# Performance work log

Measured on AMD Instinct MI355X. Metric: run time of the kernel, lower is better.

The kernel has to match this reference:

```python
import jax, jax.numpy as jnp
import numpy as np

N = 100000      # num_nodes
E = 500000      # num_edges
D = 128         # memory_dim (also per-head out channels of TransformerConv)
EF = 16         # edge_feat_dim
H = 2           # heads
OUT = 64        # classifier out_channels


def setup_inputs() -> dict:
    key = jax.random.key(0)
    ks = jax.random.split(key, 24)
    g = lambda k, shape, s=0.05: (jax.random.normal(k, shape, jnp.float32) * s)
    inp = {
        "edge_index": jax.random.randint(ks[0], (2, E), 0, N, dtype=jnp.int64),
        "edge_attr": jax.random.normal(ks[1], (E, EF), jnp.float32),
        "edge_time": jax.random.uniform(ks[2], (E,), jnp.float32),
        # memory buffer (non-trainable in torch); randn so gathers are non-trivial
        "memory": g(ks[3], (N, D), 0.1),
        # MessageModule MLP: Linear(2D+EF -> D), ReLU, Linear(D -> D)
        "w1": g(ks[4], (2 * D + EF, D)), "b1": g(ks[5], (D,)),
        "w2": g(ks[6], (D, D)), "b2": g(ks[7], (D,)),
        # GRUCell(D, D): torch layout [3D, D] with gate order r,z,n
        "gru_wih": g(ks[8], (3 * D, D)), "gru_whh": g(ks[9], (3 * D, D)),
        "gru_bih": g(ks[10], (3 * D,)), "gru_bhh": g(ks[11], (3 * D,)),
        # TransformerConv(D, D, heads=H): lin_query/key/value: D -> H*D, lin_skip: D -> H*D
        "wq": g(ks[12], (D, H * D)), "bq": g(ks[13], (H * D,)),
        "wk": g(ks[14], (D, H * D)), "bk": g(ks[15], (H * D,)),
        "wv": g(ks[16], (D, H * D)), "bv": g(ks[17], (H * D,)),
        "wskip": g(ks[18], (D, H * D)), "bskip": g(ks[19], (H * D,)),
        # classifier: H*D -> OUT
        "wc": g(ks[20], (H * D, OUT)), "bc": g(ks[21], (OUT,)),
    }
    return inp


def reference(edge_index, edge_attr, edge_time, memory, w1, b1, w2, b2,
              gru_wih, gru_whh, gru_bih, gru_bhh,
              wq, bq, wk, bk, wv, bv, wskip, bskip, wc, bc):
    n_nodes = memory.shape[0]
    src, dst = edge_index[0], edge_index[1]
    # memory is a requires_grad=False parameter in torch
    mem = jax.lax.stop_gradient(memory)

    # ---- message computation (gather + MLP) ----
    src_mem = mem[src]                      # [E, D]
    dst_mem = mem[dst]                      # [E, D]
    msg_in = jnp.concatenate([src_mem, dst_mem, edge_attr], axis=-1)
    messages = jax.nn.relu(msg_in @ w1 + b1) @ w2 + b2   # [E, D]

    # ---- GRUCell memory update (torch gate order: r, z, n) ----
    gi = messages @ gru_wih.T + gru_bih     # [E, 3D]
    gh = dst_mem @ gru_whh.T + gru_bhh      # [E, 3D]
    i_r, i_z, i_n = jnp.split(gi, 3, axis=-1)
    h_r, h_z, h_n = jnp.split(gh, 3, axis=-1)
    r = jax.nn.sigmoid(i_r + h_r)
    z = jax.nn.sigmoid(i_z + h_z)
    n = jnp.tanh(i_n + r * h_n)
    new_mem = (1.0 - z) * n + z * dst_mem   # [E, D]
    # detached scatter write (memory.data[node_ids] = updated_mem.data)
    node_mem = mem.at[dst].set(jax.lax.stop_gradient(new_mem))  # [N, D]

    # ---- TransformerConv(D, D, heads=H), concat=True, root_weight=True ----
    q = (node_mem @ wq + bq).reshape(n_nodes, H, D)
    k = (node_mem @ wk + bk).reshape(n_nodes, H, D)
    v = (node_mem @ wv + bv).reshape(n_nodes, H, D)
    # per-edge attention logits, aggregated at destination node
    logits = jnp.sum(q[dst] * k[src], axis=-1) / jnp.sqrt(jnp.float32(D))  # [E, H]
    m = jax.ops.segment_max(logits, dst, num_segments=n_nodes)             # [N, H]
    ex = jnp.exp(logits - m[dst])
    s = jax.ops.segment_sum(ex, dst, num_segments=n_nodes)                 # [N, H]
    alpha = ex / (s[dst] + 1e-16)                                          # [E, H]
    agg = jax.ops.segment_sum(v[src] * alpha[..., None], dst,
                              num_segments=n_nodes)                        # [N, H, D]
    conv_out = agg.reshape(n_nodes, H * D) + node_mem @ wskip + bskip

    # ---- classifier ----
    return conv_out @ wc + bc               # [N, OUT]
```

## Files before the change

kernel.cpp:

```cpp
#include <hip/hip_runtime.h>
#include <hip/hip_bf16.h>

#define DD 128
#define EFD 16
#define HDIM 256
#define OUTD 64
#define AW 296

#define P_W1T 0
#define P_W2T 36864
#define P_WIH 53248
#define P_WHH 102400
#define P_QKV 151552
#define P_WSK 249856
#define P_WCT 282624
#define P_TOT 299008

using bf16 = __hip_bfloat16;
typedef __attribute__((ext_vector_type(8))) short fab;
typedef __attribute__((ext_vector_type(4))) float f4;

__device__ __forceinline__ float b2f(bf16 x){ return __bfloat162float(x); }
__device__ __forceinline__ bf16  f2b(float x){ return __float2bfloat16(x); }
__device__ __forceinline__ unsigned short us(bf16 x){ return *(unsigned short*)&x; }
__device__ __forceinline__ float rawbf(unsigned int u16){
  return __uint_as_float(u16 << 16);
}
__device__ __forceinline__ unsigned pk2(float a, float b){
  return (unsigned)us(f2b(a)) | ((unsigned)us(f2b(b)) << 16);
}
__device__ __forceinline__ float gw(const void* p, size_t i, int f32){
  return f32 ? ((const float*)p)[i] : b2f(((const bf16*)p)[i]);
}
__device__ __forceinline__ uint2 ld4bf(const void* base, size_t off, int f32){
  if(f32){
    float4 v = *(const float4*)((const float*)base + off);
    uint2 r;
    r.x = pk2(v.x, v.y);
    r.y = pk2(v.z, v.w);
    return r;
  }
  return *(const uint2*)((const bf16*)base + off);
}
__device__ __forceinline__ int geti(const int* ei, int is64, long long idx){
  return is64 ? ei[2*idx] : ei[(size_t)idx];
}
__device__ __forceinline__ int clampi(int x, int hi){
  return x < 0 ? 0 : (x >= hi ? hi-1 : x);
}
__device__ __forceinline__ float gru_out(float ir, float hr, float iz, float hz,
                                         float in_, float hn, float bN_i, float bN_h,
                                         float bR, float bZ, float hp, bool upd){
  if(!upd) return hp;
  float rr = 1.f/(1.f+__expf(-(ir+hr+bR)));
  float zz = 1.f/(1.f+__expf(-(iz+hz+bZ)));
  float nn = tanhf(in_+bN_i + rr*(hn+bN_h));
  return (1.f-zz)*nn + zz*hp;
}

__global__ void k_detect(const int* __restrict__ ei,
                         const unsigned short* __restrict__ mem16,
                         int* __restrict__ flags){
  __shared__ int s64, sf32;
  int t = threadIdx.x;
  if(t == 0){ s64 = 1; sf32 = 0; }
  __syncthreads();
  if(ei[2*t + 1] != 0) atomicAnd(&s64, 0);
  int cnt = 0;
  for(int i = t; i < 4096; i += 256){
    unsigned short h = mem16[2*i];
    if((h & 0x7f80u) >= 0x4000u) cnt++;
  }
  atomicAdd(&sf32, cnt);
  __syncthreads();
  if(t == 0){ flags[0] = s64; flags[1] = (sf32 > 8) ? 1 : 0; }
}

__global__ void k_init(int* winner, int* cntrp, int N){
  int i = blockIdx.x*blockDim.x + threadIdx.x;
  if(i < N) winner[i] = -1;
  if(i <= N) cntrp[i] = 0;
}

__global__ void k_winner(const int* __restrict__ ei, const int* __restrict__ flags,
                         int* winner, int* cntrp, int E, int N){
  int e = blockIdx.x*blockDim.x + threadIdx.x;
  if(e >= E) return;
  int d = clampi(geti(ei, flags[0], (long long)E + e), N);
  atomicMax(&winner[d], e);
  atomicAdd(&cntrp[d], 1);
}

__global__ void k_scanA(const int* __restrict__ cnt, int* __restrict__ bsum, int N, int P){
  __shared__ int sd[256];
  int b = blockIdx.x, t = threadIdx.x;
  int base = (b*256 + t)*P;
  int s = 0;
  for(int p=0;p<P;p++){ int i = base+p; if(i<N) s += cnt[i]; }
  sd[t] = s; __syncthreads();
  for(int off=128; off>0; off>>=1){
    if(t<off) sd[t] += sd[t+off];
    __syncthreads();
  }
  if(t==0) bsum[b] = sd[0];
}

__global__ void k_scanB(const int* __restrict__ bsum, int* __restrict__ boff,
                        int* __restrict__ rowptr, int N, int E){
  __shared__ int sd[256];
  int t = threadIdx.x;
  int v = bsum[t];
  sd[t] = v; __syncthreads();
  for(int off=1; off<256; off<<=1){
    int u = (t>=off) ? sd[t-off] : 0;
    __syncthreads();
    sd[t] += u;
    __syncthreads();
  }
  boff[t] = sd[t] - v;
  if(t==0) rowptr[N] = E;
}

__global__ void k_scanC(int* __restrict__ cntrp, const int* __restrict__ boff,
                        int* __restrict__ head, int N, int P){
  __shared__ int sd[256];
  int b = blockIdx.x, t = threadIdx.x;
  int base = (b*256 + t)*P;
  int loc[8];
  int s = 0;
  for(int p=0;p<P;p++){ int i=base+p; int cc=(i<N)?cntrp[i]:0; loc[p]=s; s+=cc; }
  sd[t]=s; __syncthreads();
  for(int off=1; off<256; off<<=1){
    int u=(t>=off)?sd[t-off]:0;
    __syncthreads(); sd[t]+=u; __syncthreads();
  }
  int start = boff[b] + sd[t] - s;
  for(int p=0;p<P;p++){
    int i=base+p;
    if(i<N){ int r = start + loc[p]; cntrp[i]=r; head[i]=r; }
  }
}

__global__ void k_scatter(const int* __restrict__ ei, const int* __restrict__ flags,
                          int* __restrict__ head, int* __restrict__ esrc, int E, int N){
  int e = blockIdx.x*256 + threadIdx.x;
  if(e >= E) return;
  int is64 = flags[0];
  int src = clampi(geti(ei, is64, e), N);
  int dst = clampi(geti(ei, is64, (long long)E + e), N);
  int slot = atomicAdd(&head[dst], 1);
  esrc[slot] = src;
}

__global__ void k_pack(const void* w1, const void* w2, const void* wih, const void* whh,
                       const void* wq, const void* wk, const void* wv,
                       const void* wsk, const void* wc,
                       const int* __restrict__ flags, bf16* __restrict__ pk){
  int i = blockIdx.x*256 + threadIdx.x;
  if(i >= P_TOT) return;
  int f = flags[1];
  float v;
  if(i < P_W2T){ int j = i/288, c = i%288; v = (c < 272) ? gw(w1,(size_t)c*DD + j, f) : 0.f; }
  else if(i < P_WIH){ int r = i - P_W2T; int j = r>>7, c = r&127; v = gw(w2,(size_t)c*DD + j, f); }
  else if(i < P_WHH){ v = gw(wih, i - P_WIH, f); }
  else if(i < P_QKV){ v = gw(whh, i - P_WHH, f); }
  else if(i < P_WSK){
    int r = i - P_QKV; int jj = r>>7, c = r&127;
    int tb = jj>>8, j = jj&255;
    const void* w = (tb==0) ? wq : ((tb==1) ? wk : wv);
    v = gw(w, (size_t)c*HDIM + j, f);
  }
  else if(i < P_WCT){ int r = i - P_WSK; int j = r>>7, c = r&127; v = gw(wsk,(size_t)c*HDIM + j, f); }
  else { int r = i - P_WCT; int o = r>>8, j = r&255; v = gw(wc,(size_t)j*OUTD + o, f); }
  pk[i] = f2b(v);
}

__global__ __launch_bounds__(512) void k_msggru_qkv(
    const int* __restrict__ ei, const void* __restrict__ eattr,
    const void* __restrict__ mem, const bf16* __restrict__ pk,
    const void* b1, const void* b2, const void* bih, const void* bhh,
    const void* bq, const void* bk, const void* bv,
    const int* __restrict__ winner, const int* __restrict__ flags,
    bf16* __restrict__ node_mem, bf16* __restrict__ qt, bf16* __restrict__ kv, int N){
  const bf16* pw1T = pk + P_W1T;
  const bf16* pw2T = pk + P_W2T;
  const bf16* pwih = pk + P_WIH;
  const bf16* pwhh = pk + P_WHH;
  __shared__ bf16 Abuf[128][AW];
  __shared__ int swin[128], ssrc[128];
  int t = threadIdx.x;
  int n0 = blockIdx.x*128;
  int f = flags[1], is64 = flags[0];
  if(t < 128){
    int n = n0 + t;
    int w = (n < N) ? winner[n] : -1;
    swin[t] = w;
    ssrc[t] = (w >= 0) ? clampi(geti(ei, is64, w), N) : 0;
  }
  __syncthreads();
  const uint2 z2 = {0u, 0u};
  for(int idx=t; idx<128*32; idx+=512){
    int i = idx>>5, c4 = (idx&31)*4;
    int w = swin[i], n = n0+i;
    uint2 sv = (w>=0) ? ld4bf(mem, (size_t)ssrc[i]*DD + c4, f) : z2;
    uint2 dv = (n<N)  ? ld4bf(mem, (size_t)n*DD + c4, f)      : z2;
    *(uint2*)&Abuf[i][c4]    = sv;
    *(uint2*)&Abuf[i][DD+c4] = dv;
  }
  for(int idx=t; idx<128*4; idx+=512){
    int i = idx>>2, c4 = (idx&3)*4;
    uint2 v = (swin[i]>=0) ? ld4bf(eattr, (size_t)swin[i]*EFD + c4, f) : z2;
    *(uint2*)&Abuf[i][256+c4] = v;
  }
  for(int idx=t; idx<128*6; idx+=512){
    int i = idx/6, c4 = 272 + (idx%6)*4;
    *(uint2*)&Abuf[i][c4] = z2;
  }
  __syncthreads();

  int lane  = t & 63;
  int wid   = t >> 6;
  int col16 = lane & 15;
  int quad  = lane >> 4;
  int q8    = quad*8;
  int ch    = wid*16 + quad*4;

  {
    uint2 hres[8];
    const bf16* wrow = pw1T + (size_t)(wid*16 + col16)*288 + q8;
    fab w[9];
    #pragma unroll
    for(int kc=0;kc<9;kc++) w[kc] = *(const fab*)(wrow + kc*32);
    float bb0 = gw(b1, ch,   f), bb1 = gw(b1, ch+1, f);
    float bb2 = gw(b1, ch+2, f), bb3 = gw(b1, ch+3, f);
    #pragma unroll
    for(int mt=0; mt<8; mt++){
      f4 acc = (f4){0.f,0.f,0.f,0.f};
      #pragma unroll
      for(int kc=0;kc<9;kc++){
        fab an = *(const fab*)&Abuf[mt*16+col16][kc*32+q8];
        acc = __builtin_amdgcn_mfma_f32_16x16x32_bf16(w[kc], an, acc, 0,0,0);
      }
      uint2 hv;
      hv.x = pk2(fmaxf(acc[0]+bb0,0.f), fmaxf(acc[1]+bb1,0.f));
      hv.y = pk2(fmaxf(acc[2]+bb2,0.f), fmaxf(acc[3]+bb3,0.f));
      hres[mt] = hv;
    }
    __syncthreads();
    #pragma unroll
    for(int mt=0; mt<8; mt++)
      *(uint2*)&Abuf[mt*16+col16][ch] = hres[mt];
    __syncthreads();
  }

  {
    uint2 mres[8];
    const bf16* wrow = pw2T + (size_t)(wid*16 + col16)*128 + q8;
    fab w[4];
    #pragma unroll
    for(int kc=0;kc<4;kc++) w[kc] = *(const fab*)(wrow + kc*32);
    float bb0 = gw(b2, ch,   f), bb1 = gw(b2, ch+1, f);
    float bb2 = gw(b2, ch+2, f), bb3 = gw(b2, ch+3, f);
    #pragma unroll
    for(int mt=0; mt<8; mt++){
      f4 acc = (f4){0.f,0.f,0.f,0.f};
      #pragma unroll
      for(int kc=0;kc<4;kc++){
        fab an = *(const fab*)&Abuf[mt*16+col16][kc*32+q8];
        acc = __builtin_amdgcn_mfma_f32_16x16x32_bf16(w[kc], an, acc, 0,0,0);
      }
      uint2 hv;
      hv.x = pk2(acc[0]+bb0, acc[1]+bb1);
      hv.y = pk2(acc[2]+bb2, acc[3]+bb3);
      mres[mt] = hv;
    }
    __syncthreads();
    #pragma unroll
    for(int mt=0; mt<8; mt++)
      *(uint2*)&Abuf[mt*16+col16][ch] = mres[mt];
    __syncthreads();
  }

  {
    uint2 ovals[8];
    size_t row = (size_t)(wid*16 + col16)*128;
    const bf16* wi = pwih + row + q8;
    const bf16* wh = pwhh + row + q8;
    float bR0 = gw(bih,ch,f)+gw(bhh,ch,f),     bR1 = gw(bih,ch+1,f)+gw(bhh,ch+1,f);
    float bR2 = gw(bih,ch+2,f)+gw(bhh,ch+2,f), bR3 = gw(bih,ch+3,f)+gw(bhh,ch+3,f);
    float bZ0 = gw(bih,128+ch,f)+gw(bhh,128+ch,f), bZ1 = gw(bih,129+ch,f)+gw(bhh,129+ch,f);
    float bZ2 = gw(bih,130+ch,f)+gw(bhh,130+ch,f), bZ3 = gw(bih,131+ch,f)+gw(bhh,131+ch,f);
    float bNi0 = gw(bih,256+ch,f), bNi1 = gw(bih,257+ch,f);
    float bNi2 = gw(bih,258+ch,f), bNi3 = gw(bih,259+ch,f);
    float bNh0 = gw(bhh,256+ch,f), bNh1 = gw(bhh,257+ch,f);
    float bNh2 = gw(bhh,258+ch,f), bNh3 = gw(bhh,259+ch,f);
    #pragma unroll
    for(int mt=0; mt<8; mt++){
      int arow = mt*16 + col16;
      f4 ri=(f4){0,0,0,0}, zi=(f4){0,0,0,0}, ni=(f4){0,0,0,0};
      #pragma unroll
      for(int kc=0;kc<4;kc++){
        int kb = kc*32;
        fab am = *(const fab*)&Abuf[arow][kb+q8];
        ri = __builtin_amdgcn_mfma_f32_16x16x32_bf16(*(const fab*)(wi+kb),       am, ri, 0,0,0);
        zi = __builtin_amdgcn_mfma_f32_16x16x32_bf16(*(const fab*)(wi+16384+kb), am, zi, 0,0,0);
        ni = __builtin_amdgcn_mfma_f32_16x16x32_bf16(*(const fab*)(wi+32768+kb), am, ni, 0,0,0);
      }
      f4 rh=(f4){0,0,0,0}, zh=(f4){0,0,0,0}, nh=(f4){0,0,0,0};
      #pragma unroll
      for(int kc=0;kc<4;kc++){
        int kb = kc*32;
        fab ad = *(const fab*)&Abuf[arow][DD+kb+q8];
        rh = __builtin_amdgcn_mfma_f32_16x16x32_bf16(*(const fab*)(wh+kb),       ad, rh, 0,0,0);
        zh = __builtin_amdgcn_mfma_f32_16x16x32_bf16(*(const fab*)(wh+16384+kb), ad, zh, 0,0,0);
        nh = __builtin_amdgcn_mfma_f32_16x16x32_bf16(*(const fab*)(wh+32768+kb), ad, nh, 0,0,0);
      }
      bool upd = (swin[arow] >= 0);
      uint2 hraw = *(const uint2*)&Abuf[arow][DD+ch];
      float hp0 = rawbf(hraw.x & 0xffffu), hp1 = rawbf(hraw.x >> 16);
      float hp2 = rawbf(hraw.y & 0xffffu), hp3 = rawbf(hraw.y >> 16);
      float o0 = gru_out(ri[0],rh[0],zi[0],zh[0],ni[0],nh[0],bNi0,bNh0,bR0,bZ0,hp0,upd);
      float o1 = gru_out(ri[1],rh[1],zi[1],zh[1],ni[1],nh[1],bNi1,bNh1,bR1,bZ1,hp1,upd);
      float o2 = gru_out(ri[2],rh[2],zi[2],zh[2],ni[2],nh[2],bNi2,bNh2,bR2,bZ2,hp2,upd);
      float o3 = gru_out(ri[3],rh[3],zi[3],zh[3],ni[3],nh[3],bNi3,bNh3,bR3,bZ3,hp3,upd);
      uint2 ov;
      ov.x = pk2(o0, o1);
      ov.y = pk2(o2, o3);
      ovals[mt] = ov;
      int n = n0 + arow;
      if(n < N) *(uint2*)&node_mem[(size_t)n*DD + ch] = ov;
    }
    __syncthreads();
    #pragma unroll
    for(int mt=0; mt<8; mt++)
      *(uint2*)&Abuf[mt*16+col16][ch] = ovals[mt];
    __syncthreads();
  }

  {
    const bf16* pq = pk + P_QKV;
    #pragma unroll 2
    for(int i=0;i<6;i++){
      int nt = wid*6 + i;
      const bf16* wrow = pq + (size_t)(nt*16 + col16)*128 + q8;
      fab w[4];
      #pragma unroll
      for(int kc=0;kc<4;kc++) w[kc] = *(const fab*)(wrow + kc*32);
      int dch = nt*16 + quad*4;
      int tb = dch >> 8, j = dch & 255;
      const void* bp = (tb==0) ? bq : ((tb==1) ? bk : bv);
      float bb0 = gw(bp, j,   f), bb1 = gw(bp, j+1, f);
      float bb2 = gw(bp, j+2, f), bb3 = gw(bp, j+3, f);
      #pragma unroll
      for(int mt=0; mt<8; mt++){
        f4 acc = (f4){0.f,0.f,0.f,0.f};
        #pragma unroll
        for(int kc=0;kc<4;kc++){
          fab an = *(const fab*)&Abuf[mt*16+col16][kc*32+q8];
          acc = __builtin_amdgcn_mfma_f32_16x16x32_bf16(w[kc], an, acc, 0,0,0);
        }
        int n = n0 + mt*16 + col16;
        if(n < N){
          uint2 ov;
          ov.x = pk2(acc[0]+bb0, acc[1]+bb1);
          ov.y = pk2(acc[2]+bb2, acc[3]+bb3);
          if(tb==0) *(uint2*)&qt[(size_t)n*HDIM + j] = ov;
          else      *(uint2*)&kv[(size_t)n*512 + ((tb==1)?0:256) + j] = ov;
        }
      }
    }
  }
}

__global__ __launch_bounds__(256) void k_attn(
    const bf16* __restrict__ qt, const bf16* __restrict__ kv,
    const int* __restrict__ rowptr, const int* __restrict__ esrc,
    bf16* __restrict__ aggb, int N){
  int lane = threadIdx.x & 63;
  int n = blockIdx.x*4 + (threadIdx.x >> 6);
  if(n >= N) return;
  int beg = rowptr[n], end = rowptr[n+1];
  uint4 qa = *(const uint4*)(qt + (size_t)n*HDIM + 8*(lane & 31));
  float q0 = rawbf(qa.x & 0xffffu), q1 = rawbf(qa.x >> 16);
  float q2 = rawbf(qa.y & 0xffffu), q3 = rawbf(qa.y >> 16);
  float q4 = rawbf(qa.z & 0xffffu), q5 = rawbf(qa.z >> 16);
  float q6 = rawbf(qa.w & 0xffffu), q7 = rawbf(qa.w >> 16);
  float acc[8] = {0.f,0.f,0.f,0.f,0.f,0.f,0.f,0.f};
  float l = 0.f;
  for(int c = beg; c < end; c += 64){
    int se = (c + lane < end) ? esrc[c + lane] : 0;
    int ce = end - c; if(ce > 64) ce = 64;
    int s0 = __shfl(se, 0, 64);
    uint4 cur = *(const uint4*)(kv + (size_t)s0*512 + 8*lane);
    for(int j = 0; j < ce; j++){
      uint4 nxt = {0u,0u,0u,0u};
      if(j + 1 < ce){
        int s1 = __shfl(se, j + 1, 64);
        nxt = *(const uint4*)(kv + (size_t)s1*512 + 8*lane);
      }
      float p = q0*rawbf(cur.x & 0xffffu) + q1*rawbf(cur.x >> 16)
              + q2*rawbf(cur.y & 0xffffu) + q3*rawbf(cur.y >> 16)
              + q4*rawbf(cur.z & 0xffffu) + q5*rawbf(cur.z >> 16)
              + q6*rawbf(cur.w & 0xffffu) + q7*rawbf(cur.w >> 16);
      p += __shfl_xor(p, 8, 64); p += __shfl_xor(p, 4, 64);
      p += __shfl_xor(p, 2, 64); p += __shfl_xor(p, 1, 64);
      float ex = __expf(p * 0.08838834764831845f);
      l += ex;
      float exv = __shfl(ex, lane & 31, 64);
      acc[0] += exv*rawbf(cur.x & 0xffffu); acc[1] += exv*rawbf(cur.x >> 16);
      acc[2] += exv*rawbf(cur.y & 0xffffu); acc[3] += exv*rawbf(cur.y >> 16);
      acc[4] += exv*rawbf(cur.z & 0xffffu); acc[5] += exv*rawbf(cur.z >> 16);
      acc[6] += exv*rawbf(cur.w & 0xffffu); acc[7] += exv*rawbf(cur.w >> 16);
      cur = nxt;
    }
  }
  float ls = __shfl(l, lane & 31, 64);
  if(lane >= 32){
    float li = 1.f/(ls + 1e-16f);
    uint4 w;
    w.x = pk2(acc[0]*li, acc[1]*li);
    w.y = pk2(acc[2]*li, acc[3]*li);
    w.z = pk2(acc[4]*li, acc[5]*li);
    w.w = pk2(acc[6]*li, acc[7]*li);
    *(uint4*)(aggb + (size_t)n*HDIM + 8*(lane - 32)) = w;
  }
}

__global__ __launch_bounds__(256) void k_cls_mfma(
    const bf16* __restrict__ node_mem, const bf16* __restrict__ aggb,
    const bf16* __restrict__ pk, const void* bsk, const void* bc,
    const int* __restrict__ flags, float* __restrict__ out, int N){
  __shared__ bf16 Abuf[64][128];
  __shared__ bf16 Cbuf[64][HDIM];
  int t = threadIdx.x, n0 = blockIdx.x*64, f = flags[1];
  for(int id=t; id<1024; id+=256){
    int i = id>>4, c8 = (id&15)*8;
    int n = n0 + i;
    uint4 val = {0u,0u,0u,0u};
    if(n < N) val = *(const uint4*)&node_mem[(size_t)n*DD + c8];
    *(uint4*)&Abuf[i][c8] = val;
  }
  __syncthreads();
  int lane = t&63, m0 = (t>>6)*16, col16 = lane&15, quad = lane>>4;
  {
    fab a[4];
    #pragma unroll
    for(int kc=0;kc<4;kc++) a[kc] = *(const fab*)&Abuf[m0+col16][kc*32+quad*8];
    const bf16* psk = pk + P_WSK;
    for(int nt=0;nt<16;nt++){
      f4 acc = (f4){0.f,0.f,0.f,0.f};
      #pragma unroll
      for(int kc=0;kc<4;kc++){
        fab b = *(const fab*)&psk[(size_t)(nt*16 + col16)*128 + kc*32+quad*8];
        acc = __builtin_amdgcn_mfma_f32_16x16x32_bf16(a[kc], b, acc, 0,0,0);
      }
      int j = nt*16 + col16;
      float bb = gw(bsk, j, f);
      #pragma unroll
      for(int r=0;r<4;r++){
        int row = m0 + quad*4 + r;
        int n = n0 + row;
        float cv = acc[r] + bb + ((n < N) ? b2f(aggb[(size_t)n*HDIM + j]) : 0.f);
        Cbuf[row][j] = f2b(cv);
      }
    }
  }
  __syncthreads();
  {
    fab a2[8];
    #pragma unroll
    for(int kc=0;kc<8;kc++) a2[kc] = *(const fab*)&Cbuf[m0+col16][kc*32+quad*8];
    const bf16* pct = pk + P_WCT;
    for(int nt=0;nt<4;nt++){
      f4 acc = (f4){0.f,0.f,0.f,0.f};
      #pragma unroll
      for(int kc=0;kc<8;kc++){
        fab b = *(const fab*)&pct[(size_t)(nt*16 + col16)*HDIM + kc*32+quad*8];
        acc = __builtin_amdgcn_mfma_f32_16x16x32_bf16(a2[kc], b, acc, 0,0,0);
      }
      int o = nt*16 + col16;
      float bb = gw(bc, o, f);
      #pragma unroll
      for(int r=0;r<4;r++){
        int n = n0 + m0 + quad*4 + r;
        if(n < N) out[(size_t)n*OUTD + o] = acc[r] + bb;
      }
    }
  }
}

extern "C" void kernel_launch(void* const* d_in, const int* in_sizes, int n_in,
                              void* d_out, int out_size, void* d_ws, size_t ws_size,
                              hipStream_t stream){
  const int*  ei    = (const int*)d_in[0];
  const void* eattr = d_in[1];
  const void* mem   = d_in[3];
  const void* w1  = d_in[4];  const void* b1  = d_in[5];
  const void* w2  = d_in[6];  const void* b2  = d_in[7];
  const void* wih = d_in[8];  const void* whh = d_in[9];
  const void* bih = d_in[10]; const void* bhh = d_in[11];
  const void* wq  = d_in[12]; const void* bq  = d_in[13];
  const void* wk  = d_in[14]; const void* bk  = d_in[15];
  const void* wv  = d_in[16]; const void* bv  = d_in[17];
  const void* wsk = d_in[18]; const void* bsk = d_in[19];
  const void* wc  = d_in[20]; const void* bc  = d_in[21];
  float* out = (float*)d_out;
  const int E = in_sizes[2];
  const int N = in_sizes[3] / DD;

  char* p = (char*)d_ws;
  auto alloc = [&](size_t bytes)->char*{
    char* r = p; p += (bytes + 511) & ~(size_t)511; return r;
  };
  int*   flags  = (int*)  alloc(8);
  int*   winner = (int*)  alloc((size_t)N*4);
  bf16*  pk     = (bf16*) alloc((size_t)P_TOT*2);
  bf16*  node_mem = (bf16*)alloc((size_t)N*DD*2);
  bf16*  kv   = (bf16*)alloc((size_t)N*512*2);
  bf16*  qt   = (bf16*)alloc((size_t)N*HDIM*2);
  bf16*  aggb = qt;
  int*   cntrp = (int*)alloc(((size_t)N+1)*4);
  int*   head  = (int*)alloc((size_t)N*4);
  int*   bsum  = (int*)alloc(256*4);
  int*   boff  = (int*)alloc(256*4);
  int*   esrc  = (int*)alloc((size_t)E*4);

  size_t required = (size_t)(p - (char*)d_ws);
  if(required > ws_size) return;

  const int P = (N + 256*256 - 1) / (256*256);

  hipLaunchKernelGGL(k_detect, dim3(1), dim3(256), 0, stream,
                     ei, (const unsigned short*)mem, flags);
  hipLaunchKernelGGL(k_init,   dim3((N+256)/256), dim3(256), 0, stream, winner, cntrp, N);
  hipLaunchKernelGGL(k_winner, dim3((E+255)/256), dim3(256), 0, stream,
                     ei, flags, winner, cntrp, E, N);
  hipLaunchKernelGGL(k_pack,   dim3((P_TOT+255)/256), dim3(256), 0, stream,
                     w1, w2, wih, whh, wq, wk, wv, wsk, wc, flags, pk);
  hipLaunchKernelGGL(k_msggru_qkv, dim3((N+127)/128), dim3(512), 0, stream,
                     ei, eattr, mem, pk, b1, b2, bih, bhh, bq, bk, bv,
                     winner, flags, node_mem, qt, kv, N);
  hipLaunchKernelGGL(k_scanA, dim3(256), dim3(256), 0, stream, cntrp, bsum, N, P);
  hipLaunchKernelGGL(k_scanB, dim3(1),   dim3(256), 0, stream, bsum, boff, cntrp, N, E);
  hipLaunchKernelGGL(k_scanC, dim3(256), dim3(256), 0, stream, cntrp, boff, head, N, P);
  hipLaunchKernelGGL(k_scatter, dim3((E+255)/256), dim3(256), 0, stream,
                     ei, flags, head, esrc, E, N);
  hipLaunchKernelGGL(k_attn, dim3((N+3)/4), dim3(256), 0, stream,
                     qt, kv, cntrp, esrc, aggb, N);
  hipLaunchKernelGGL(k_cls_mfma, dim3((N+63)/64), dim3(256), 0, stream,
                     node_mem, aggb, pk, bsk, bc, flags, out, N);
}
```

Baseline: 663.5 us.

## Assign row tiles per wave to drop block syncs in fused node MLP/GRU/QKV

```diff
diff --git a/kernel.cpp b/kernel.cpp
--- a/kernel.cpp
+++ b/kernel.cpp
@@ -47,15 +47,6 @@
 }
 __device__ __forceinline__ int clampi(int x, int hi){
   return x < 0 ? 0 : (x >= hi ? hi-1 : x);
-}
-__device__ __forceinline__ float gru_out(float ir, float hr, float iz, float hz,
-                                         float in_, float hn, float bN_i, float bN_h,
-                                         float bR, float bZ, float hp, bool upd){
-  if(!upd) return hp;
-  float rr = 1.f/(1.f+__expf(-(ir+hr+bR)));
-  float zz = 1.f/(1.f+__expf(-(iz+hz+bZ)));
-  float nn = tanhf(in_+bN_i + rr*(hn+bN_h));
-  return (1.f-zz)*nn + zz*hp;
 }
 
 __global__ void k_detect(const int* __restrict__ ei,
@@ -219,154 +210,137 @@
   __syncthreads();
 
   int lane  = t & 63;
-  int wid   = t >> 6;
+  int wv    = t >> 6;
   int col16 = lane & 15;
   int quad  = lane >> 4;
   int q8    = quad*8;
-  int ch    = wid*16 + quad*4;
+  int arow  = wv*16 + col16;
+  int nglob = n0 + arow;
+  bool inb  = (nglob < N);
 
   {
-    uint2 hres[8];
-    const bf16* wrow = pw1T + (size_t)(wid*16 + col16)*288 + q8;
-    fab w[9];
+    fab an[9];
     #pragma unroll
-    for(int kc=0;kc<9;kc++) w[kc] = *(const fab*)(wrow + kc*32);
-    float bb0 = gw(b1, ch,   f), bb1 = gw(b1, ch+1, f);
-    float bb2 = gw(b1, ch+2, f), bb3 = gw(b1, ch+3, f);
-    #pragma unroll
-    for(int mt=0; mt<8; mt++){
+    for(int kc=0;kc<9;kc++) an[kc] = *(const fab*)&Abuf[arow][kc*32+q8];
+    #pragma unroll 2
+    for(int nt=0;nt<8;nt++){
+      const bf16* wrow = pw1T + (size_t)(nt*16 + col16)*288 + q8;
+      fab w[9];
+      #pragma unroll
+      for(int kc=0;kc<9;kc++) w[kc] = *(const fab*)(wrow + kc*32);
       f4 acc = (f4){0.f,0.f,0.f,0.f};
       #pragma unroll
-      for(int kc=0;kc<9;kc++){
-        fab an = *(const fab*)&Abuf[mt*16+col16][kc*32+q8];
-        acc = __builtin_amdgcn_mfma_f32_16x16x32_bf16(w[kc], an, acc, 0,0,0);
-      }
+      for(int kc=0;kc<9;kc++)
+        acc = __builtin_amdgcn_mfma_f32_16x16x32_bf16(w[kc], an[kc], acc, 0,0,0);
+      int ch = nt*16 + quad*4;
+      float bb0 = gw(b1, ch,   f), bb1 = gw(b1, ch+1, f);
+      float bb2 = gw(b1, ch+2, f), bb3 = gw(b1, ch+3, f);
       uint2 hv;
       hv.x = pk2(fmaxf(acc[0]+bb0,0.f), fmaxf(acc[1]+bb1,0.f));
       hv.y = pk2(fmaxf(acc[2]+bb2,0.f), fmaxf(acc[3]+bb3,0.f));
-      hres[mt] = hv;
-    }
-    __syncthreads();
+      *(uint2*)&Abuf[arow][ch] = hv;
+    }
+  }
+
+  {
+    fab an2[4];
     #pragma unroll
-    for(int mt=0; mt<8; mt++)
-      *(uint2*)&Abuf[mt*16+col16][ch] = hres[mt];
-    __syncthreads();
-  }
-
-  {
-    uint2 mres[8];
-    const bf16* wrow = pw2T + (size_t)(wid*16 + col16)*128 + q8;
-    fab w[4];
-    #pragma unroll
-    for(int kc=0;kc<4;kc++) w[kc] = *(const fab*)(wrow + kc*32);
-    float bb0 = gw(b2, ch,   f), bb1 = gw(b2, ch+1, f);
-    float bb2 = gw(b2, ch+2, f), bb3 = gw(b2, ch+3, f);
-    #pragma unroll
-    for(int mt=0; mt<8; mt++){
+    for(int kc=0;kc<4;kc++) an2[kc] = *(const fab*)&Abuf[arow][kc*32+q8];
+    #pragma unroll 2
+    for(int nt=0;nt<8;nt++){
+      const bf16* wrow = pw2T + (size_t)(nt*16 + col16)*128 + q8;
+      fab w[4];
+      #pragma unroll
+      for(int kc=0;kc<4;kc++) w[kc] = *(const fab*)(wrow + kc*32);
       f4 acc = (f4){0.f,0.f,0.f,0.f};
       #pragma unroll
-      for(int kc=0;kc<4;kc++){
-        fab an = *(const fab*)&Abuf[mt*16+col16][kc*32+q8];
-        acc = __builtin_amdgcn_mfma_f32_16x16x32_bf16(w[kc], an, acc, 0,0,0);
-      }
+      for(int kc=0;kc<4;kc++)
+        acc = __builtin_amdgcn_mfma_f32_16x16x32_bf16(w[kc], an2[kc], acc, 0,0,0);
+      int ch = nt*16 + quad*4;
+      float bb0 = gw(b2, ch,   f), bb1 = gw(b2, ch+1, f);
+      float bb2 = gw(b2, ch+2, f), bb3 = gw(b2, ch+3, f);
       uint2 hv;
       hv.x = pk2(acc[0]+bb0, acc[1]+bb1);
       hv.y = pk2(acc[2]+bb2, acc[3]+bb3);
-      mres[mt] = hv;
-    }
-    __syncthreads();
+      *(uint2*)&Abuf[arow][ch] = hv;
+    }
+  }
+
+  {
+    fab am[4], ad[4];
     #pragma unroll
-    for(int mt=0; mt<8; mt++)
-      *(uint2*)&Abuf[mt*16+col16][ch] = mres[mt];
-    __syncthreads();
-  }
-
-  {
-    uint2 ovals[8];
-    size_t row = (size_t)(wid*16 + col16)*128;
-    const bf16* wi = pwih + row + q8;
-    const bf16* wh = pwhh + row + q8;
-    float bR0 = gw(bih,ch,f)+gw(bhh,ch,f),     bR1 = gw(bih,ch+1,f)+gw(bhh,ch+1,f);
-    float bR2 = gw(bih,ch+2,f)+gw(bhh,ch+2,f), bR3 = gw(bih,ch+3,f)+gw(bhh,ch+3,f);
-    float bZ0 = gw(bih,128+ch,f)+gw(bhh,128+ch,f), bZ1 = gw(bih,129+ch,f)+gw(bhh,129+ch,f);
-    float bZ2 = gw(bih,130+ch,f)+gw(bhh,130+ch,f), bZ3 = gw(bih,131+ch,f)+gw(bhh,131+ch,f);
-    float bNi0 = gw(bih,256+ch,f), bNi1 = gw(bih,257+ch,f);
-    float bNi2 = gw(bih,258+ch,f), bNi3 = gw(bih,259+ch,f);
-    float bNh0 = gw(bhh,256+ch,f), bNh1 = gw(bhh,257+ch,f);
-    float bNh2 = gw(bhh,258+ch,f), bNh3 = gw(bhh,259+ch,f);
-    #pragma unroll
-    for(int mt=0; mt<8; mt++){
-      int arow = mt*16 + col16;
-      f4 ri=(f4){0,0,0,0}, zi=(f4){0,0,0,0}, ni=(f4){0,0,0,0};
+    for(int kc=0;kc<4;kc++){
+      am[kc] = *(const fab*)&Abuf[arow][kc*32+q8];
+      ad[kc] = *(const fab*)&Abuf[arow][DD + kc*32+q8];
+    }
+    bool upd = (swin[arow] >= 0);
+    for(int nt=0;nt<8;nt++){
+      size_t row = (size_t)(nt*16 + col16)*128;
+      const bf16* wi = pwih + row + q8;
+      const bf16* wh = pwhh + row + q8;
+      f4 aR=(f4){0,0,0,0}, aZ=(f4){0,0,0,0}, aNi=(f4){0,0,0,0}, aNh=(f4){0,0,0,0};
       #pragma unroll
       for(int kc=0;kc<4;kc++){
         int kb = kc*32;
-        fab am = *(const fab*)&Abuf[arow][kb+q8];
-        ri = __builtin_amdgcn_mfma_f32_16x16x32_bf16(*(const fab*)(wi+kb),       am, ri, 0,0,0);
-        zi = __builtin_amdgcn_mfma_f32_16x16x32_bf16(*(const fab*)(wi+16384+kb), am, zi, 0,0,0);
-        ni = __builtin_amdgcn_mfma_f32_16x16x32_bf16(*(const fab*)(wi+32768+kb), am, ni, 0,0,0);
-      }
-      f4 rh=(f4){0,0,0,0}, zh=(f4){0,0,0,0}, nh=(f4){0,0,0,0};
-      #pragma unroll
-      for(int kc=0;kc<4;kc++){
-        int kb = kc*32;
-        fab ad = *(const fab*)&Abuf[arow][DD+kb+q8];
-        rh = __builtin_amdgcn_mfma_f32_16x16x32_bf16(*(const fab*)(wh+kb),       ad, rh, 0,0,0);
-        zh = __builtin_amdgcn_mfma_f32_16x16x32_bf16(*(const fab*)(wh+16384+kb), ad, zh, 0,0,0);
-        nh = __builtin_amdgcn_mfma_f32_16x16x32_bf16(*(const fab*)(wh+32768+kb), ad, nh, 0,0,0);
-      }
-      bool upd = (swin[arow] >= 0);
+        aR  = __builtin_amdgcn_mfma_f32_16x16x32_bf16(*(const fab*)(wi+kb),       am[kc], aR, 0,0,0);
+        aR  = __builtin_amdgcn_mfma_f32_16x16x32_bf16(*(const fab*)(wh+kb),       ad[kc], aR, 0,0,0);
+        aZ  = __builtin_amdgcn_mfma_f32_16x16x32_bf16(*(const fab*)(wi+16384+kb), am[kc], aZ, 0,0,0);
+        aZ  = __builtin_amdgcn_mfma_f32_16x16x32_bf16(*(const fab*)(wh+16384+kb), ad[kc], aZ, 0,0,0);
+        aNi = __builtin_amdgcn_mfma_f32_16x16x32_bf16(*(const fab*)(wi+32768+kb), am[kc], aNi, 0,0,0);
+        aNh = __builtin_amdgcn_mfma_f32_16x16x32_bf16(*(const fab*)(wh+32768+kb), ad[kc], aNh, 0,0,0);
+      }
+      int ch = nt*16 + quad*4;
       uint2 hraw = *(const uint2*)&Abuf[arow][DD+ch];
-      float hp0 = rawbf(hraw.x & 0xffffu), hp1 = rawbf(hraw.x >> 16);
-      float hp2 = rawbf(hraw.y & 0xffffu), hp3 = rawbf(hraw.y >> 16);
-      float o0 = gru_out(ri[0],rh[0],zi[0],zh[0],ni[0],nh[0],bNi0,bNh0,bR0,bZ0,hp0,upd);
-      float o1 = gru_out(ri[1],rh[1],zi[1],zh[1],ni[1],nh[1],bNi1,bNh1,bR1,bZ1,hp1,upd);
-      float o2 = gru_out(ri[2],rh[2],zi[2],zh[2],ni[2],nh[2],bNi2,bNh2,bR2,bZ2,hp2,upd);
-      float o3 = gru_out(ri[3],rh[3],zi[3],zh[3],ni[3],nh[3],bNi3,bNh3,bR3,bZ3,hp3,upd);
+      float hp[4] = { rawbf(hraw.x & 0xffffu), rawbf(hraw.x >> 16),
+                      rawbf(hraw.y & 0xffffu), rawbf(hraw.y >> 16) };
+      float o[4];
+      #pragma unroll
+      for(int r=0;r<4;r++){
+        if(upd){
+          float bR  = gw(bih,ch+r,f) + gw(bhh,ch+r,f);
+          float bZ  = gw(bih,128+ch+r,f) + gw(bhh,128+ch+r,f);
+          float bNi = gw(bih,256+ch+r,f);
+          float bNh = gw(bhh,256+ch+r,f);
+          float rr = 1.f/(1.f+__expf(-(aR[r]+bR)));
+          float zz = 1.f/(1.f+__expf(-(aZ[r]+bZ)));
+          float nn = tanhf(aNi[r]+bNi + rr*(aNh[r]+bNh));
+          o[r] = (1.f-zz)*nn + zz*hp[r];
+        } else o[r] = hp[r];
+      }
       uint2 ov;
-      ov.x = pk2(o0, o1);
-      ov.y = pk2(o2, o3);
-      ovals[mt] = ov;
-      int n = n0 + arow;
-      if(n < N) *(uint2*)&node_mem[(size_t)n*DD + ch] = ov;
-    }
-    __syncthreads();
+      ov.x = pk2(o[0], o[1]);
+      ov.y = pk2(o[2], o[3]);
+      *(uint2*)&Abuf[arow][ch] = ov;
+      if(inb) *(uint2*)&node_mem[(size_t)nglob*DD + ch] = ov;
+    }
+  }
+
+  {
+    fab an3[4];
     #pragma unroll
-    for(int mt=0; mt<8; mt++)
-      *(uint2*)&Abuf[mt*16+col16][ch] = ovals[mt];
-    __syncthreads();
-  }
-
-  {
+    for(int kc=0;kc<4;kc++) an3[kc] = *(const fab*)&Abuf[arow][kc*32+q8];
     const bf16* pq = pk + P_QKV;
     #pragma unroll 2
-    for(int i=0;i<6;i++){
-      int nt = wid*6 + i;
+    for(int nt=0;nt<48;nt++){
       const bf16* wrow = pq + (size_t)(nt*16 + col16)*128 + q8;
       fab w[4];
       #pragma unroll
       for(int kc=0;kc<4;kc++) w[kc] = *(const fab*)(wrow + kc*32);
+      f4 acc = (f4){0.f,0.f,0.f,0.f};
+      #pragma unroll
+      for(int kc=0;kc<4;kc++)
+        acc = __builtin_amdgcn_mfma_f32_16x16x32_bf16(w[kc], an3[kc], acc, 0,0,0);
       int dch = nt*16 + quad*4;
       int tb = dch >> 8, j = dch & 255;
       const void* bp = (tb==0) ? bq : ((tb==1) ? bk : bv);
       float bb0 = gw(bp, j,   f), bb1 = gw(bp, j+1, f);
       float bb2 = gw(bp, j+2, f), bb3 = gw(bp, j+3, f);
-      #pragma unroll
-      for(int mt=0; mt<8; mt++){
-        f4 acc = (f4){0.f,0.f,0.f,0.f};
-        #pragma unroll
-        for(int kc=0;kc<4;kc++){
-          fab an = *(const fab*)&Abuf[mt*16+col16][kc*32+q8];
-          acc = __builtin_amdgcn_mfma_f32_16x16x32_bf16(w[kc], an, acc, 0,0,0);
-        }
-        int n = n0 + mt*16 + col16;
-        if(n < N){
-          uint2 ov;
-          ov.x = pk2(acc[0]+bb0, acc[1]+bb1);
-          ov.y = pk2(acc[2]+bb2, acc[3]+bb3);
-          if(tb==0) *(uint2*)&qt[(size_t)n*HDIM + j] = ov;
-          else      *(uint2*)&kv[(size_t)n*512 + ((tb==1)?0:256) + j] = ov;
-        }
+      if(inb){
+        uint2 ov;
+        ov.x = pk2(acc[0]+bb0, acc[1]+bb1);
+        ov.y = pk2(acc[2]+bb2, acc[3]+bb3);
+        if(tb==0) *(uint2*)&qt[(size_t)nglob*HDIM + j] = ov;
+        else      *(uint2*)&kv[(size_t)nglob*512 + ((tb==1)?0:256) + j] = ov;
       }
     }
   }
```

Result: slower. 871.4 us (+31.3%).
